# Kernel tuning notes

Hardware: AMD Instinct MI355X
Metric: run time of the kernel (lower is better)

## Reference

```python
import jax, jax.numpy as jnp
import numpy as np

N = 50000
E = 800000
NODE_IN, EDGE_IN, HID, OUT, L = 32, 16, 128, 128, 2


def _layer_norm(h, g, b, eps=1e-5):
    mu = jnp.mean(h, axis=-1, keepdims=True)
    var = jnp.var(h, axis=-1, keepdims=True)
    return (h - mu) * jax.lax.rsqrt(var + eps) * g + b


def setup_inputs() -> dict:
    key = jax.random.key(0)
    ks = jax.random.split(key, 20)
    s = lambda k, shape, fan: jax.random.normal(k, shape, jnp.float32) * (1.0 / np.sqrt(fan))
    return {
        "x": jax.random.normal(ks[0], (N, NODE_IN), jnp.float32),
        "edge_index": jax.random.randint(ks[1], (2, E), 0, N, jnp.int64),
        "edge_attr": jax.random.normal(ks[2], (E, EDGE_IN), jnp.float32),
        "enc_W": s(ks[3], (NODE_IN, HID), NODE_IN),
        "enc_b": jnp.zeros((HID,), jnp.float32),
        "enc_g": jnp.ones((HID,), jnp.float32),
        "enc_beta": jnp.zeros((HID,), jnp.float32),
        "msg_W1": s(ks[4], (L, 2 * HID + EDGE_IN, HID), 2 * HID + EDGE_IN),
        "msg_b1": jnp.zeros((L, HID), jnp.float32),
        "msg_W2": s(ks[5], (L, HID, HID), HID),
        "msg_b2": jnp.zeros((L, HID), jnp.float32),
        "upd_W1": s(ks[6], (L, 2 * HID, HID), 2 * HID),
        "upd_b1": jnp.zeros((L, HID), jnp.float32),
        "upd_W2": s(ks[7], (L, HID, HID), HID),
        "upd_b2": jnp.zeros((L, HID), jnp.float32),
        "ln_g": jnp.ones((L, HID), jnp.float32),
        "ln_beta": jnp.zeros((L, HID), jnp.float32),
        "head_W": s(ks[8], (HID, OUT), HID),
        "head_b": jnp.zeros((OUT,), jnp.float32),
    }


def reference(x, edge_index, edge_attr, enc_W, enc_b, enc_g, enc_beta,
              msg_W1, msg_b1, msg_W2, msg_b2, upd_W1, upd_b1, upd_W2, upd_b2,
              ln_g, ln_beta, head_W, head_b):
    src = edge_index[0]  # x_j (source)
    tgt = edge_index[1]  # x_i (target, aggregation index)
    n = x.shape[0]

    # node encoder: Linear -> ReLU -> LayerNorm
    h = jax.nn.relu(x @ enc_W + enc_b)
    h = _layer_norm(h, enc_g, enc_beta)

    # per-edge incoming-degree for mean aggregation (isolated nodes -> 0)
    cnt = jax.ops.segment_sum(jnp.ones((tgt.shape[0],), h.dtype), tgt, num_segments=n)
    denom = jnp.maximum(cnt, 1.0)[:, None]

    for l in range(L):
        x_i = h[tgt]                                 # [E, HID]
        x_j = h[src]                                 # [E, HID]
        msg_in = jnp.concatenate([x_i, x_j, edge_attr], axis=-1)  # [E, 2H+Ed]
        m = jax.nn.relu(msg_in @ msg_W1[l] + msg_b1[l]) @ msg_W2[l] + msg_b2[l]
        aggr = jax.ops.segment_sum(m, tgt, num_segments=n) / denom  # mean
        upd_in = jnp.concatenate([h, aggr], axis=-1)
        out = jax.nn.relu(upd_in @ upd_W1[l] + upd_b1[l]) @ upd_W2[l] + upd_b2[l]
        h = _layer_norm(h + out, ln_g[l], ln_beta[l])

    return h @ head_W + head_b
```

## Files before the change

kernel.cpp:

```cpp
#include <hip/hip_runtime.h>
#include <hip/hip_bf16.h>
#include <stdint.h>

#define N_NODES 50000
#define N_EDGES 800000
#define NL 2

#define KS2 136
#define KSU 264
#define ESTR 132

typedef __bf16 bf16x8 __attribute__((ext_vector_type(8)));
typedef float f32x4 __attribute__((ext_vector_type(4)));

__device__ __forceinline__ f32x4 mfma_bf16(uint4 a, uint4 b, f32x4 c) {
    return __builtin_amdgcn_mfma_f32_16x16x32_bf16(
        __builtin_bit_cast(bf16x8, a), __builtin_bit_cast(bf16x8, b), c, 0, 0, 0);
}

__device__ __forceinline__ unsigned short f2b(float f) {
    union { float f; unsigned u; } v; v.f = f;
    unsigned r = v.u + 0x7FFFu + ((v.u >> 16) & 1u);
    return (unsigned short)(r >> 16);
}

__device__ __forceinline__ float b2f(unsigned short u) {
    union { unsigned u; float f; } v; v.u = ((unsigned)u) << 16; return v.f;
}
__device__ __forceinline__ float b2f_lo(unsigned u) {
    union { unsigned u; float f; } v; v.u = u << 16; return v.f;
}
__device__ __forceinline__ float b2f_hi(unsigned u) {
    union { unsigned u; float f; } v; v.u = u & 0xFFFF0000u; return v.f;
}
__device__ __forceinline__ unsigned pk2(unsigned short a, unsigned short b) {
    return (unsigned)a | ((unsigned)b << 16);
}

template<int KSTEPS, int BSTR>
__device__ __forceinline__ void gemm4(const unsigned short* aLane,
                                      const unsigned short* bLane, f32x4 acc[4]) {
#pragma unroll
    for (int kc = 0; kc < KSTEPS; kc++) {
        uint4 a = *(const uint4*)(aLane + kc * 32);
#pragma unroll
        for (int ct = 0; ct < 4; ct++) {
            uint4 b = *(const uint4*)(bLane + (size_t)ct * 16 * BSTR + kc * 32);
            acc[ct] = mfma_bf16(a, b, acc[ct]);
        }
    }
}

template<int KSTEPS, int ASTR, int BSTR>
__device__ __forceinline__ void gemm_1x4(const unsigned short* aLane,
                                         const unsigned short* bLane,
                                         f32x4 acc[4]) {
#pragma unroll
    for (int kc = 0; kc < KSTEPS; kc++) {
        uint4 b0 = *(const uint4*)(bLane + kc * 32);
#pragma unroll
        for (int rt = 0; rt < 4; rt++) {
            uint4 a = *(const uint4*)(aLane + (size_t)rt * 16 * ASTR + kc * 32);
            acc[rt] = mfma_bf16(a, b0, acc[rt]);
        }
    }
}

template<int KSTEPS, int ASTR, int BSTR>
__device__ __forceinline__ void gemm_2x4(const unsigned short* aLane,
                                         const unsigned short* bLane,
                                         f32x4 acc[4][2]) {
#pragma unroll
    for (int kc = 0; kc < KSTEPS; kc++) {
        uint4 b0 = *(const uint4*)(bLane + kc * 32);
        uint4 b1 = *(const uint4*)(bLane + (size_t)16 * BSTR + kc * 32);
#pragma unroll
        for (int rt = 0; rt < 4; rt++) {
            uint4 a = *(const uint4*)(aLane + (size_t)rt * 16 * ASTR + kc * 32);
            acc[rt][0] = mfma_bf16(a, b0, acc[rt][0]);
            acc[rt][1] = mfma_bf16(a, b1, acc[rt][1]);
        }
    }
}

__global__ void prep_kernel(const float* __restrict__ mW1,
                            const float* __restrict__ uW1, const float* __restrict__ uW2,
                            const float* __restrict__ hW,
                            unsigned short* __restrict__ wab, unsigned short* __restrict__ w1cp,
                            unsigned short* __restrict__ u1t, unsigned short* __restrict__ u2t,
                            unsigned short* __restrict__ ht) {
    int i = blockIdx.x * 256 + threadIdx.x;
    const int SA = NL * 256 * 136;
    const int SC = NL * 128 * 32;
    const int SU = NL * 128 * KSU;
    const int S3 = NL * 128 * KS2;
    const int S4 = 128 * KS2;
    if (i < SA) {
        int l = i / (256 * 136), r = i % (256 * 136), j = r / 136, k = r % 136;
        float v = 0.f;
        if (k < 128)
            v = (j < 128) ? mW1[((size_t)l * 272 + k) * 128 + j]
                          : mW1[((size_t)l * 272 + 128 + k) * 128 + (j - 128)];
        wab[i] = f2b(v);
        return;
    }
    i -= SA;
    if (i < SC) {
        int l = i / (128 * 32), r = i % (128 * 32), j = r / 32, k = r % 32;
        w1cp[i] = (k < 16) ? f2b(mW1[((size_t)l * 272 + 256 + k) * 128 + j]) : (unsigned short)0;
        return;
    }
    i -= SC;
    if (i < SU) {
        int l = i / (128 * KSU), r = i % (128 * KSU), n = r / KSU, k = r % KSU;
        if (k < 128)       u1t[i] = f2b(uW1[((size_t)l * 256 + k) * 128 + n]);
        else if (k >= 256) u1t[i] = 0;
        return;
    }
    i -= SU;
    if (i < S3) {
        int l = i / (128 * KS2), r = i % (128 * KS2), n = r / KS2, k = r % KS2;
        u2t[i] = (k < 128) ? f2b(uW2[((size_t)l * 128 + k) * 128 + n]) : (unsigned short)0;
        return;
    }
    i -= S3;
    if (i < S4) {
        int n = i / KS2, k = i % KS2;
        ht[i] = (k < 128) ? f2b(hW[(size_t)k * 128 + n]) : (unsigned short)0;
    }
}

__global__ void prep2_kernel(const float* __restrict__ mW2, const float* __restrict__ uW1,
                             unsigned short* __restrict__ u1t) {
    __shared__ float w2row[128];
    const int l = blockIdx.x >> 7, j = blockIdx.x & 127;
    const int n = threadIdx.x;
    w2row[n] = mW2[((size_t)l * 128 + j) * 128 + n];
    __syncthreads();
    float s = 0.f;
#pragma unroll 8
    for (int c = 0; c < 128; c++)
        s += w2row[c] * uW1[((size_t)l * 256 + 128 + c) * 128 + n];
    u1t[(size_t)l * 128 * KSU + (size_t)n * KSU + 128 + j] = f2b(s);
}

__global__ void prep3_kernel(const float* __restrict__ mb2, const float* __restrict__ uW1,
                             float* __restrict__ bfold) {
    const int l = blockIdx.x;
    const int n = threadIdx.x;
    float s = 0.f;
#pragma unroll 8
    for (int c = 0; c < 128; c++)
        s += mb2[l * 128 + c] * uW1[((size_t)l * 256 + 128 + c) * 128 + n];
    bfold[l * 128 + n] = s;
}

__global__ __launch_bounds__(512, 6) void encnode_kernel(
        const float* __restrict__ x, const float* __restrict__ W,
        const float* __restrict__ b, const float* __restrict__ g, const float* __restrict__ bet,
        const unsigned short* __restrict__ wab, const float* __restrict__ b1,
        unsigned short* __restrict__ hb,
        unsigned short* __restrict__ Tb, unsigned short* __restrict__ Sb) {
    __shared__ __align__(16) unsigned short Ah[64 * KS2];
    __shared__ float xs[64 * 33];
    __shared__ __align__(16) float Ws[32 * 128];
    const int t = threadIdx.x;
    const int n0 = blockIdx.x * 64;

    {
        const int m = t >> 3, q = t & 7;
        const int nd = n0 + m;
        float4 v = {0.f, 0.f, 0.f, 0.f};
        if (nd < N_NODES) v = *(const float4*)(x + (size_t)nd * 32 + q * 4);
        xs[m * 33 + q * 4 + 0] = v.x;
        xs[m * 33 + q * 4 + 1] = v.y;
        xs[m * 33 + q * 4 + 2] = v.z;
        xs[m * 33 + q * 4 + 3] = v.w;
    }
    {
        const float4* s = (const float4*)W;
        float4* d = (float4*)Ws;
        d[t * 2] = s[t * 2];
        d[t * 2 + 1] = s[t * 2 + 1];
    }
    __syncthreads();

    const int r = t >> 3, q8 = t & 7;
    const int node = n0 + r;
    const bool valid = (node < N_NODES);

    float vbuf[16];
#pragma unroll
    for (int j = 0; j < 16; j++) vbuf[j] = b[q8 + 8 * j];
    for (int k = 0; k < 32; k++) {
        const float xv = xs[r * 33 + k];
#pragma unroll
        for (int j = 0; j < 16; j++)
            vbuf[j] += xv * Ws[k * 128 + q8 + 8 * j];
    }
#pragma unroll
    for (int j = 0; j < 16; j++) vbuf[j] = fmaxf(vbuf[j], 0.f);

    {
        float s = 0.f, ss = 0.f;
#pragma unroll
        for (int j = 0; j < 16; j++) { s += vbuf[j]; ss += vbuf[j] * vbuf[j]; }
        s += __shfl_xor(s, 1); ss += __shfl_xor(ss, 1);
        s += __shfl_xor(s, 2); ss += __shfl_xor(ss, 2);
        s += __shfl_xor(s, 4); ss += __shfl_xor(ss, 4);
        const float mu = s * (1.0f / 128.0f);
        const float var = ss * (1.0f / 128.0f) - mu * mu;
        const float rs = rsqrtf(var + 1e-5f);
#pragma unroll
        for (int j = 0; j < 16; j++) {
            const int col = q8 + 8 * j;
            const float v = (vbuf[j] - mu) * rs * g[col] + bet[col];
            Ah[r * KS2 + col] = valid ? f2b(v) : (unsigned short)0;
        }
    }
    __syncthreads();

    {
        const int m = t >> 3, q = t & 7;
        const int nd = n0 + m;
        if (nd < N_NODES) {
            const uint4* srow = (const uint4*)(Ah + (size_t)m * KS2);
            uint4* drow = (uint4*)(hb + (size_t)nd * 128);
            drow[q * 2] = srow[q * 2];
            drow[q * 2 + 1] = srow[q * 2 + 1];
        }
    }

    const int wv = t >> 6, lane = t & 63, lr = lane & 15, lq = lane >> 4;
    const int cbn = wv * 32;
    const f32x4 z4 = {0.f, 0.f, 0.f, 0.f};
    f32x4 accn[4][2];
#pragma unroll
    for (int i = 0; i < 4; i++) { accn[i][0] = z4; accn[i][1] = z4; }
    gemm_2x4<4, KS2, KS2>(Ah + lr * KS2 + lq * 8,
                          wab + (size_t)(cbn + lr) * KS2 + lq * 8, accn);
#pragma unroll
    for (int ct = 0; ct < 2; ct++) {
        const int j = cbn + ct * 16 + lr;
        const float bias = (j < 128) ? b1[j] : 0.f;
#pragma unroll
        for (int rt = 0; rt < 4; rt++) {
#pragma unroll
            for (int r2 = 0; r2 < 4; r2++) {
                const int node2 = n0 + rt * 16 + lq * 4 + r2;
                if (node2 < N_NODES) {
                    const float v = accn[rt][ct][r2] + bias;
                    if (j < 128) Tb[(size_t)node2 * 128 + j] = f2b(v);
                    else         Sb[(size_t)node2 * 128 + (j - 128)] = f2b(v);
                }
            }
        }
    }
}

__global__ void hist_kernel(const int* __restrict__ tgt, int* __restrict__ hist) {
    int i = blockIdx.x * 256 + threadIdx.x;
    atomicAdd(hist + tgt[i], 1);
}

__global__ void scan1_kernel(const int* __restrict__ hist, int* __restrict__ incl,
                             int* __restrict__ blksum) {
    __shared__ int buf[256];
    const int t = threadIdx.x;
    const int i = blockIdx.x * 256 + t;
    int v = (i < N_NODES) ? hist[i] : 0;
    buf[t] = v; __syncthreads();
#pragma unroll
    for (int d = 1; d < 256; d <<= 1) {
        int x = (t >= d) ? buf[t - d] : 0;
        __syncthreads();
        buf[t] += x;
        __syncthreads();
    }
    if (i < N_NODES) incl[i] = buf[t];
    if (t == 255) blksum[blockIdx.x] = buf[255];
}

__global__ void scan2_kernel(int* __restrict__ blksum, int nblk) {
    __shared__ int buf[256];
    const int t = threadIdx.x;
    int v = (t < nblk) ? blksum[t] : 0;
    buf[t] = v; __syncthreads();
#pragma unroll
    for (int d = 1; d < 256; d <<= 1) {
        int x = (t >= d) ? buf[t - d] : 0;
        __syncthreads();
        buf[t] += x;
        __syncthreads();
    }
    if (t < nblk) blksum[t] = buf[t];
}

__global__ void scan3_kernel(int* __restrict__ incl, const int* __restrict__ blksum,
                             const int* __restrict__ hist) {
    const int i = blockIdx.x * 256 + threadIdx.x;
    if (i >= N_NODES) return;
    const int b = blockIdx.x;
    const int base = (b > 0) ? blksum[b - 1] : 0;
    incl[i] = incl[i] + base - hist[i];
}

__global__ void scatterp_kernel(const int* __restrict__ src, const int* __restrict__ tgt,
                                int* __restrict__ cursor, uint2* __restrict__ permst) {
    const int e = blockIdx.x * 256 + threadIdx.x;
    const int tg = tgt[e];
    const int p = atomicAdd(cursor + tg, 1);
    permst[p] = make_uint2((unsigned)e, ((unsigned)src[e] << 16) | (unsigned)tg);
}

__global__ __launch_bounds__(256) void gather_kernel(
        const uint2* __restrict__ permst, const float* __restrict__ ea,
        unsigned int* __restrict__ sST, unsigned short* __restrict__ eabS) {
    const int p = blockIdx.x * 256 + threadIdx.x;
    const uint2 v = permst[p];
    sST[p] = v.y;
    const float4* s = (const float4*)(ea + (size_t)v.x * 16);
    ushort4* d = (ushort4*)(eabS + (size_t)p * 16);
#pragma unroll
    for (int i = 0; i < 4; i++) {
        float4 f = s[i];
        d[i] = make_ushort4(f2b(f.x), f2b(f.y), f2b(f.z), f2b(f.w));
    }
}

__global__ __launch_bounds__(256, 8) void edge_kernel(
        const unsigned short* __restrict__ eabS,
        const unsigned int* __restrict__ sST,
        const unsigned short* __restrict__ w1cp,
        const unsigned short* __restrict__ Tb, const unsigned short* __restrict__ Sb,
        float* __restrict__ aggr) {
    __shared__ __align__(16) float Es[32 * ESTR];
    __shared__ int sT[64];
    __shared__ int sS[64];

    const int t = threadIdx.x;
    const int e0 = blockIdx.x * 64;
    if (t < 64) {
        const unsigned v = sST[e0 + t];
        sT[t] = (int)(v & 0xFFFFu);
        sS[t] = (int)(v >> 16);
    }
    __syncthreads();

    const int wv = t >> 6, lane = t & 63, lr = lane & 15, lq = lane >> 4;
    const int rtw = (wv >> 1) * 16;
    const int cbw = (wv & 1) * 64;
    const int m = t & 31, c8b = t >> 5;
    const f32x4 z4 = {0.f, 0.f, 0.f, 0.f};

    unsigned long long bmask;
    {
        const int l = t & 63;
        const int a = sT[l];
        const int b = (l > 0) ? sT[l - 1] : a;
        bmask = __ballot(a != b);
    }

    uint4 t0a, t0b, s0a, s0b;
    {
        const unsigned short* Tr = Tb + (size_t)sT[m] * 128;
        const unsigned short* Sr = Sb + (size_t)sS[m] * 128;
        t0a = *(const uint4*)(Tr + c8b * 8);
        t0b = *(const uint4*)(Tr + c8b * 8 + 64);
        s0a = *(const uint4*)(Sr + c8b * 8);
        s0b = *(const uint4*)(Sr + c8b * 8 + 64);
    }

    float s = 0.f;
    bool first = true;

    {
        uint4 a = {0, 0, 0, 0};
        if (lq < 2)
            a = *(const uint4*)(eabS + (size_t)(e0 + rtw + lr) * 16 + lq * 8);
        f32x4 acc[4];
#pragma unroll
        for (int ct = 0; ct < 4; ct++) {
            uint4 b = *(const uint4*)(w1cp + (cbw + ct * 16 + lr) * 32 + lq * 8);
            acc[ct] = mfma_bf16(a, b, z4);
        }
#pragma unroll
        for (int ct = 0; ct < 4; ct++) {
            const int col = cbw + ct * 16 + lr;
#pragma unroll
            for (int r = 0; r < 4; r++)
                Es[(rtw + lq * 4 + r) * ESTR + col] = acc[ct][r];
        }
    }
    __syncthreads();

    uint4 t1a, t1b, s1a, s1b;
    {
        float* Erow = Es + m * ESTR;
        float4* EA = (float4*)(Erow + c8b * 8);
        float4* EB = (float4*)(Erow + c8b * 8 + 64);
        float4 ea0 = EA[0], ea1 = EA[1];
        ea0.x = fmaxf(ea0.x + b2f_lo(t0a.x) + b2f_lo(s0a.x), 0.f);
        ea0.y = fmaxf(ea0.y + b2f_hi(t0a.x) + b2f_hi(s0a.x), 0.f);
        ea0.z = fmaxf(ea0.z + b2f_lo(t0a.y) + b2f_lo(s0a.y), 0.f);
        ea0.w = fmaxf(ea0.w + b2f_hi(t0a.y) + b2f_hi(s0a.y), 0.f);
        ea1.x = fmaxf(ea1.x + b2f_lo(t0a.z) + b2f_lo(s0a.z), 0.f);
        ea1.y = fmaxf(ea1.y + b2f_hi(t0a.z) + b2f_hi(s0a.z), 0.f);
        ea1.z = fmaxf(ea1.z + b2f_lo(t0a.w) + b2f_lo(s0a.w), 0.f);
        ea1.w = fmaxf(ea1.w + b2f_hi(t0a.w) + b2f_hi(s0a.w), 0.f);
        EA[0] = ea0; EA[1] = ea1;
        float4 eb0 = EB[0], eb1 = EB[1];
        eb0.x = fmaxf(eb0.x + b2f_lo(t0b.x) + b2f_lo(s0b.x), 0.f);
        eb0.y = fmaxf(eb0.y + b2f_hi(t0b.x) + b2f_hi(s0b.x), 0.f);
        eb0.z = fmaxf(eb0.z + b2f_lo(t0b.y) + b2f_lo(s0b.y), 0.f);
        eb0.w = fmaxf(eb0.w + b2f_hi(t0b.y) + b2f_hi(s0b.y), 0.f);
        eb1.x = fmaxf(eb1.x + b2f_lo(t0b.z) + b2f_lo(s0b.z), 0.f);
        eb1.y = fmaxf(eb1.y + b2f_hi(t0b.z) + b2f_hi(s0b.z), 0.f);
        eb1.z = fmaxf(eb1.z + b2f_lo(t0b.w) + b2f_lo(s0b.w), 0.f);
        eb1.w = fmaxf(eb1.w + b2f_hi(t0b.w) + b2f_hi(s0b.w), 0.f);
        EB[0] = eb0; EB[1] = eb1;

        const unsigned short* Tr = Tb + (size_t)sT[32 + m] * 128;
        const unsigned short* Sr = Sb + (size_t)sS[32 + m] * 128;
        t1a = *(const uint4*)(Tr + c8b * 8);
        t1b = *(const uint4*)(Tr + c8b * 8 + 64);
        s1a = *(const uint4*)(Sr + c8b * 8);
        s1b = *(const uint4*)(Sr + c8b * 8 + 64);
    }
    __syncthreads();

    if (t < 128) {
        const int c = t;
        const unsigned mh = (unsigned)bmask;
#pragma unroll
        for (int i8 = 0; i8 < 4; i8++) {
            float v[8];
#pragma unroll
            for (int j = 0; j < 8; j++) v[j] = Es[(i8 * 8 + j) * ESTR + c];
#pragma unroll
            for (int j = 0; j < 8; j++) {
                const int i = i8 * 8 + j;
                if (mh & (1u << i)) {
                    float* dst = aggr + (size_t)sT[i - 1] * 128 + c;
                    if (first) { atomicAdd(dst, s); first = false; }
                    else       { *dst = s; }
                    s = 0.f;
                }
                s += v[j];
            }
        }
    }
    __syncthreads();

    {
        uint4 a = {0, 0, 0, 0};
        if (lq < 2)
            a = *(const uint4*)(eabS + (size_t)(e0 + 32 + rtw + lr) * 16 + lq * 8);
        f32x4 acc[4];
#pragma unroll
        for (int ct = 0; ct < 4; ct++) {
            uint4 b = *(const uint4*)(w1cp + (cbw + ct * 16 + lr) * 32 + lq * 8);
            acc[ct] = mfma_bf16(a, b, z4);
        }
#pragma unroll
        for (int ct = 0; ct < 4; ct++) {
            const int col = cbw + ct * 16 + lr;
#pragma unroll
            for (int r = 0; r < 4; r++)
                Es[(rtw + lq * 4 + r) * ESTR + col] = acc[ct][r];
        }
    }
    __syncthreads();

    {
        float* Erow = Es + m * ESTR;
        float4* EA = (float4*)(Erow + c8b * 8);
        float4* EB = (float4*)(Erow + c8b * 8 + 64);
        float4 ea0 = EA[0], ea1 = EA[1];
        ea0.x = fmaxf(ea0.x + b2f_lo(t1a.x) + b2f_lo(s1a.x), 0.f);
        ea0.y = fmaxf(ea0.y + b2f_hi(t1a.x) + b2f_hi(s1a.x), 0.f);
        ea0.z = fmaxf(ea0.z + b2f_lo(t1a.y) + b2f_lo(s1a.y), 0.f);
        ea0.w = fmaxf(ea0.w + b2f_hi(t1a.y) + b2f_hi(s1a.y), 0.f);
        ea1.x = fmaxf(ea1.x + b2f_lo(t1a.z) + b2f_lo(s1a.z), 0.f);
        ea1.y = fmaxf(ea1.y + b2f_hi(t1a.z) + b2f_hi(s1a.z), 0.f);
        ea1.z = fmaxf(ea1.z + b2f_lo(t1a.w) + b2f_lo(s1a.w), 0.f);
        ea1.w = fmaxf(ea1.w + b2f_hi(t1a.w) + b2f_hi(s1a.w), 0.f);
        EA[0] = ea0; EA[1] = ea1;
        float4 eb0 = EB[0], eb1 = EB[1];
        eb0.x = fmaxf(eb0.x + b2f_lo(t1b.x) + b2f_lo(s1b.x), 0.f);
        eb0.y = fmaxf(eb0.y + b2f_hi(t1b.x) + b2f_hi(s1b.x), 0.f);
        eb0.z = fmaxf(eb0.z + b2f_lo(t1b.y) + b2f_lo(s1b.y), 0.f);
        eb0.w = fmaxf(eb0.w + b2f_hi(t1b.y) + b2f_hi(s1b.y), 0.f);
        eb1.x = fmaxf(eb1.x + b2f_lo(t1b.z) + b2f_lo(s1b.z), 0.f);
        eb1.y = fmaxf(eb1.y + b2f_hi(t1b.z) + b2f_hi(s1b.z), 0.f);
        eb1.z = fmaxf(eb1.z + b2f_lo(t1b.w) + b2f_lo(s1b.w), 0.f);
        eb1.w = fmaxf(eb1.w + b2f_hi(t1b.w) + b2f_hi(s1b.w), 0.f);
        EB[0] = eb0; EB[1] = eb1;
    }
    __syncthreads();

    if (t < 128) {
        const int c = t;
        const unsigned mh = (unsigned)(bmask >> 32);
#pragma unroll
        for (int i8 = 0; i8 < 4; i8++) {
            float v[8];
#pragma unroll
            for (int j = 0; j < 8; j++) v[j] = Es[(i8 * 8 + j) * ESTR + c];
#pragma unroll
            for (int j = 0; j < 8; j++) {
                const int i = i8 * 8 + j;
                if (mh & (1u << i)) {
                    float* dst = aggr + (size_t)sT[32 + i - 1] * 128 + c;
                    if (first) { atomicAdd(dst, s); first = false; }
                    else       { *dst = s; }
                    s = 0.f;
                }
                s += v[j];
            }
        }
        atomicAdd(aggr + (size_t)sT[63] * 128 + c, s);
    }
}

__global__ __launch_bounds__(512, 6) void upd_kernel(
        const unsigned short* __restrict__ hb_in,
        const float* __restrict__ aggr, const int* __restrict__ hist,
        const unsigned short* __restrict__ u1t, const unsigned short* __restrict__ u2t,
        const float* __restrict__ b1, const float* __restrict__ bf,
        const float* __restrict__ b2,
        const float* __restrict__ g, const float* __restrict__ bet,
        unsigned short* __restrict__ hb_out,
        const unsigned short* __restrict__ wabn, const float* __restrict__ b1n,
        unsigned short* __restrict__ Tb, unsigned short* __restrict__ Sb,
        const unsigned short* __restrict__ ht, const float* __restrict__ hbias,
        float* __restrict__ out, const int mode) {
    __shared__ __align__(16) char smemA[64 * KSU * 2];
    __shared__ float sF[64];
    unsigned short* As = (unsigned short*)smemA;
    float* LNb = (float*)smemA;

    const int t = threadIdx.x;
    const int n0 = blockIdx.x * 64;
    {
        const int m = t >> 3, q = t & 7;
        const int node = n0 + m;
        unsigned short* row = As + m * KSU;
        if (node < N_NODES) {
            const uint4* ph = (const uint4*)(hb_in + (size_t)node * 128);
            uint4* d0 = (uint4*)row;
            d0[q * 2] = ph[q * 2];
            d0[q * 2 + 1] = ph[q * 2 + 1];
            const int cntv = hist[node];
            if (q == 0) sF[m] = (cntv > 0) ? 1.f : 0.f;
            const float rden = 1.0f / fmaxf((float)cntv, 1.0f);
            const float4* pa = (const float4*)(aggr + (size_t)node * 128 + q * 16);
            ushort4* d1 = (ushort4*)(row + 128 + q * 16);
#pragma unroll
            for (int i = 0; i < 4; i++) {
                float4 v = pa[i];
                d1[i] = make_ushort4(f2b(v.x * rden), f2b(v.y * rden),
                                     f2b(v.z * rden), f2b(v.w * rden));
            }
            if (q == 0) { uint4 z{0, 0, 0, 0}; ((uint4*)(row + 256))[0] = z; }
        } else {
            if (q == 0) sF[m] = 0.f;
            uint4 z{0, 0, 0, 0};
            uint4* d = (uint4*)row;
            for (int i = q; i < 33; i += 8) d[i] = z;
        }
    }
    __syncthreads();

    const int wv = t >> 6, lane = t & 63, lr = lane & 15, lq = lane >> 4;
    const int cb16 = wv * 16;
    const f32x4 z4 = {0.f, 0.f, 0.f, 0.f};

    f32x4 acc[4];
#pragma unroll
    for (int i = 0; i < 4; i++) acc[i] = z4;
    gemm_1x4<8, KSU, KSU>(As + lr * KSU + lq * 8,
                          u1t + (size_t)(cb16 + lr) * KSU + lq * 8, acc);
    __syncthreads();

    {
        const int col = cb16 + lr;
        const float bv = b1[col];
        const float bfv = bf[col];
#pragma unroll
        for (int rt = 0; rt < 4; rt++) {
#pragma unroll
            for (int r = 0; r < 4; r++) {
                const int ml = rt * 16 + lq * 4 + r;
                float v = fmaxf(acc[rt][r] + bv + sF[ml] * bfv, 0.f);
                As[ml * KSU + 128 + col] = f2b(v);
            }
        }
    }
    __syncthreads();

    f32x4 acc2[4];
#pragma unroll
    for (int i = 0; i < 4; i++) acc2[i] = z4;
    gemm_1x4<4, KSU, KS2>(As + lr * KSU + 128 + lq * 8,
                          u2t + (size_t)(cb16 + lr) * KS2 + lq * 8, acc2);
    __syncthreads();

    float hres[4][4];
    {
        const int colr = cb16 + lr;
#pragma unroll
        for (int rt = 0; rt < 4; rt++)
#pragma unroll
            for (int r = 0; r < 4; r++)
                hres[rt][r] = b2f(As[(rt * 16 + lq * 4 + r) * KSU + colr]);
    }
    __syncthreads();

    {
        const int col = cb16 + lr;
        const float bv = b2[col];
#pragma unroll
        for (int rt = 0; rt < 4; rt++) {
#pragma unroll
            for (int r = 0; r < 4; r++) {
                const int ml = rt * 16 + lq * 4 + r;
                LNb[ml * 132 + col] = acc2[rt][r] + bv + hres[rt][r];
            }
        }
    }
    __syncthreads();

    const int r = t >> 3, c0 = (t & 7) * 16;
    const int node = n0 + r;
    const bool valid = (node < N_NODES);
    float vbuf[16];
    if (valid) {
        float s = 0.f, ss = 0.f;
#pragma unroll
        for (int i = 0; i < 16; i++) {
            const float v = LNb[r * 132 + c0 + i];
            vbuf[i] = v;
            s += v; ss += v * v;
        }
        s += __shfl_xor(s, 1); ss += __shfl_xor(ss, 1);
        s += __shfl_xor(s, 2); ss += __shfl_xor(ss, 2);
        s += __shfl_xor(s, 4); ss += __shfl_xor(ss, 4);
        const float mu = s * (1.0f / 128.0f);
        const float var = ss * (1.0f / 128.0f) - mu * mu;
        const float rs = rsqrtf(var + 1e-5f);
#pragma unroll
        for (int i = 0; i < 16; i++) {
            const int j = c0 + i;
            vbuf[i] = (vbuf[i] - mu) * rs * g[j] + bet[j];
        }
    }
    __syncthreads();

    unsigned short* Ah = (unsigned short*)smemA;
    {
        unsigned short hb16[16];
#pragma unroll
        for (int i = 0; i < 16; i++) hb16[i] = valid ? f2b(vbuf[i]) : (unsigned short)0;
        uint4* arow = (uint4*)(Ah + (size_t)r * KS2 + c0);
#pragma unroll
        for (int k8 = 0; k8 < 2; k8++)
            arow[k8] = make_uint4(pk2(hb16[k8 * 8 + 0], hb16[k8 * 8 + 1]),
                                  pk2(hb16[k8 * 8 + 2], hb16[k8 * 8 + 3]),
                                  pk2(hb16[k8 * 8 + 4], hb16[k8 * 8 + 5]),
                                  pk2(hb16[k8 * 8 + 6], hb16[k8 * 8 + 7]));
        if (mode == 2 && valid) {
            uint4* drow = (uint4*)(hb_out + (size_t)node * 128 + c0);
#pragma unroll
            for (int k8 = 0; k8 < 2; k8++)
                drow[k8] = make_uint4(pk2(hb16[k8 * 8 + 0], hb16[k8 * 8 + 1]),
                                      pk2(hb16[k8 * 8 + 2], hb16[k8 * 8 + 3]),
                                      pk2(hb16[k8 * 8 + 4], hb16[k8 * 8 + 5]),
                                      pk2(hb16[k8 * 8 + 6], hb16[k8 * 8 + 7]));
        }
    }
    __syncthreads();

    if (mode == 1) {
        const int m0 = (wv & 3) * 16;
        const int cblk = (wv >> 2) * 64;
        f32x4 hacc[4];
#pragma unroll
        for (int i = 0; i < 4; i++) hacc[i] = z4;
        gemm4<4, KS2>(Ah + (size_t)(m0 + lr) * KS2 + lq * 8,
                      ht + (size_t)(cblk + lr) * KS2 + lq * 8, hacc);
#pragma unroll
        for (int ct = 0; ct < 4; ct++) {
            const int col = cblk + ct * 16 + lr;
            const float bv = hbias[col];
#pragma unroll
            for (int r2 = 0; r2 < 4; r2++) {
                const int node2 = n0 + m0 + lq * 4 + r2;
                if (node2 < N_NODES) out[(size_t)node2 * 128 + col] = hacc[ct][r2] + bv;
            }
        }
    } else {
        const int cbn = wv * 32;
        f32x4 accn[4][2];
#pragma unroll
        for (int i = 0; i < 4; i++) { accn[i][0] = z4; accn[i][1] = z4; }
        gemm_2x4<4, KS2, KS2>(Ah + lr * KS2 + lq * 8,
                              wabn + (size_t)(cbn + lr) * KS2 + lq * 8, accn);
#pragma unroll
        for (int ct = 0; ct < 2; ct++) {
            const int j = cbn + ct * 16 + lr;
            const float bias = (j < 128) ? b1n[j] : 0.f;
#pragma unroll
            for (int rt = 0; rt < 4; rt++) {
#pragma unroll
                for (int r2 = 0; r2 < 4; r2++) {
                    const int node2 = n0 + rt * 16 + lq * 4 + r2;
                    if (node2 < N_NODES) {
                        const float v = accn[rt][ct][r2] + bias;
                        if (j < 128) Tb[(size_t)node2 * 128 + j] = f2b(v);
                        else         Sb[(size_t)node2 * 128 + (j - 128)] = f2b(v);
                    }
                }
            }
        }
    }
}

extern "C" void kernel_launch(void* const* d_in, const int* in_sizes, int n_in,
                              void* d_out, int out_size, void* d_ws, size_t ws_size,
                              hipStream_t stream) {
    const float* x       = (const float*)d_in[0];
    const int*   ei      = (const int*)d_in[1];
    const float* ea      = (const float*)d_in[2];
    const float* encW    = (const float*)d_in[3];
    const float* encb    = (const float*)d_in[4];
    const float* encg    = (const float*)d_in[5];
    const float* encbeta = (const float*)d_in[6];
    const float* msgW1   = (const float*)d_in[7];
    const float* msgb1   = (const float*)d_in[8];
    const float* msgW2   = (const float*)d_in[9];
    const float* msgb2   = (const float*)d_in[10];
    const float* updW1   = (const float*)d_in[11];
    const float* updb1   = (const float*)d_in[12];
    const float* updW2   = (const float*)d_in[13];
    const float* updb2   = (const float*)d_in[14];
    const float* lng     = (const float*)d_in[15];
    const float* lnbeta  = (const float*)d_in[16];
    const float* headW   = (const float*)d_in[17];
    const float* headb   = (const float*)d_in[18];

    char* w = (char*)d_ws;
    size_t off = 0;
    auto nxt = [&](size_t bytes) -> void* {
        void* p = w + off;
        off = (off + bytes + 255) & ~(size_t)255;
        return p;
    };
    unsigned short* hb    = (unsigned short*)nxt((size_t)N_NODES * 128 * 2);
    float*          aggr  = (float*)nxt((size_t)N_NODES * 128 * 4);
    unsigned short* Tb    = (unsigned short*)nxt((size_t)N_NODES * 128 * 2);
    unsigned short* Sb    = (unsigned short*)nxt((size_t)N_NODES * 128 * 2);
    unsigned short* eabS  = (unsigned short*)nxt((size_t)N_EDGES * 16 * 2);
    unsigned int*   sST   = (unsigned int*)nxt((size_t)N_EDGES * 4);
    int*            hist  = (int*)nxt((size_t)N_NODES * 4);
    int*            incl  = (int*)nxt((size_t)N_NODES * 4);
    int*            blksum= (int*)nxt(256 * 4);
    unsigned short* wab   = (unsigned short*)nxt((size_t)NL * 256 * 136 * 2);
    unsigned short* w1cp  = (unsigned short*)nxt((size_t)NL * 128 * 32 * 2);
    unsigned short* u1t   = (unsigned short*)nxt((size_t)NL * 128 * KSU * 2);
    unsigned short* u2t   = (unsigned short*)nxt((size_t)NL * 128 * KS2 * 2);
    unsigned short* ht    = (unsigned short*)nxt((size_t)128 * KS2 * 2);
    float*          bfold = (float*)nxt((size_t)NL * 128 * 4);

    uint2*          permst = (uint2*)aggr;

    const int NBLK = (N_NODES + 255) / 256;
    const int PREP_N = NL * 256 * 136 + NL * 128 * 32 + NL * 128 * KSU
                     + NL * 128 * KS2 + 128 * KS2;

    hipMemsetAsync(hist, 0, (size_t)N_NODES * 4, stream);
    prep_kernel<<<(PREP_N + 255) / 256, 256, 0, stream>>>(msgW1, updW1, updW2, headW,
                                                          wab, w1cp, u1t, u2t, ht);
    prep2_kernel<<<NL * 128, 128, 0, stream>>>(msgW2, updW1, u1t);
    prep3_kernel<<<NL, 128, 0, stream>>>(msgb2, updW1, bfold);
    encnode_kernel<<<782, 512, 0, stream>>>(x, encW, encb, encg, encbeta,
                                            wab, msgb1, hb, Tb, Sb);
    hist_kernel<<<3125, 256, 0, stream>>>(ei + N_EDGES, hist);
    scan1_kernel<<<NBLK, 256, 0, stream>>>(hist, incl, blksum);
    scan2_kernel<<<1, 256, 0, stream>>>(blksum, NBLK);
    scan3_kernel<<<NBLK, 256, 0, stream>>>(incl, blksum, hist);
    scatterp_kernel<<<3125, 256, 0, stream>>>(ei, ei + N_EDGES, incl, permst);
    gather_kernel<<<3125, 256, 0, stream>>>(permst, ea, sST, eabS);

    for (int l = 0; l < NL; l++) {
        hipMemsetAsync(aggr, 0, (size_t)N_NODES * 128 * 4, stream);
        edge_kernel<<<12500, 256, 0, stream>>>(eabS, sST,
                                               w1cp + (size_t)l * 128 * 32,
                                               Tb, Sb, aggr);
        upd_kernel<<<782, 512, 0, stream>>>(hb, aggr, hist,
                                            u1t + (size_t)l * 128 * KSU,
                                            u2t + (size_t)l * 128 * KS2,
                                            updb1 + l * 128, bfold + l * 128,
                                            updb2 + l * 128,
                                            lng + l * 128, lnbeta + l * 128,
                                            hb,
                                            wab + (size_t)(l + 1 < NL ? l + 1 : 0) * 256 * 136,
                                            msgb1 + (l + 1 < NL ? l + 1 : 0) * 128,
                                            Tb, Sb,
                                            ht, headb, (float*)d_out,
                                            (l == NL - 1) ? 1 : 2);
    }
}
```

Measured before the change: 500.4 us.

## Keep node state in fp32 and halve node tile to 32 rows per block

The node hidden state buffer moves from bf16 to fp32, so the residual add in the update LayerNorm uses full-precision h held in registers rather than a bf16 copy read back from shared memory. Node kernels now process 32 nodes per 512-thread block instead of 64, which doubles the grid and reduces shared memory per block so more blocks fit per CU. In exchange, the h buffer traffic doubles and each block does less MFMA work against the same weight loads, lowering weight reuse.

New measurement: 478.7 us (median of 2 runs). 4.3% less time.

```diff
diff --git a/kernel.cpp b/kernel.cpp
--- a/kernel.cpp
+++ b/kernel.cpp
@@ -24,9 +24,6 @@
     return (unsigned short)(r >> 16);
 }
 
-__device__ __forceinline__ float b2f(unsigned short u) {
-    union { unsigned u; float f; } v; v.u = ((unsigned)u) << 16; return v.f;
-}
 __device__ __forceinline__ float b2f_lo(unsigned u) {
     union { unsigned u; float f; } v; v.u = u << 16; return v.f;
 }
@@ -37,45 +34,31 @@
     return (unsigned)a | ((unsigned)b << 16);
 }
 
-template<int KSTEPS, int BSTR>
-__device__ __forceinline__ void gemm4(const unsigned short* aLane,
-                                      const unsigned short* bLane, f32x4 acc[4]) {
-#pragma unroll
-    for (int kc = 0; kc < KSTEPS; kc++) {
-        uint4 a = *(const uint4*)(aLane + kc * 32);
-#pragma unroll
-        for (int ct = 0; ct < 4; ct++) {
-            uint4 b = *(const uint4*)(bLane + (size_t)ct * 16 * BSTR + kc * 32);
-            acc[ct] = mfma_bf16(a, b, acc[ct]);
-        }
-    }
-}
-
-template<int KSTEPS, int ASTR, int BSTR>
-__device__ __forceinline__ void gemm_1x4(const unsigned short* aLane,
+template<int RT, int KSTEPS, int ASTR, int BSTR>
+__device__ __forceinline__ void gemm_1xR(const unsigned short* aLane,
                                          const unsigned short* bLane,
-                                         f32x4 acc[4]) {
+                                         f32x4 acc[RT]) {
 #pragma unroll
     for (int kc = 0; kc < KSTEPS; kc++) {
         uint4 b0 = *(const uint4*)(bLane + kc * 32);
 #pragma unroll
-        for (int rt = 0; rt < 4; rt++) {
+        for (int rt = 0; rt < RT; rt++) {
             uint4 a = *(const uint4*)(aLane + (size_t)rt * 16 * ASTR + kc * 32);
             acc[rt] = mfma_bf16(a, b0, acc[rt]);
         }
     }
 }
 
-template<int KSTEPS, int ASTR, int BSTR>
-__device__ __forceinline__ void gemm_2x4(const unsigned short* aLane,
+template<int RT, int KSTEPS, int ASTR, int BSTR>
+__device__ __forceinline__ void gemm_2xR(const unsigned short* aLane,
                                          const unsigned short* bLane,
-                                         f32x4 acc[4][2]) {
+                                         f32x4 acc[RT][2]) {
 #pragma unroll
     for (int kc = 0; kc < KSTEPS; kc++) {
         uint4 b0 = *(const uint4*)(bLane + kc * 32);
         uint4 b1 = *(const uint4*)(bLane + (size_t)16 * BSTR + kc * 32);
 #pragma unroll
-        for (int rt = 0; rt < 4; rt++) {
+        for (int rt = 0; rt < RT; rt++) {
             uint4 a = *(const uint4*)(aLane + (size_t)rt * 16 * ASTR + kc * 32);
             acc[rt][0] = mfma_bf16(a, b0, acc[rt][0]);
             acc[rt][1] = mfma_bf16(a, b1, acc[rt][1]);
@@ -155,27 +138,25 @@
     bfold[l * 128 + n] = s;
 }
 
-__global__ __launch_bounds__(512, 6) void encnode_kernel(
+__global__ __launch_bounds__(512, 8) void encnode_kernel(
         const float* __restrict__ x, const float* __restrict__ W,
         const float* __restrict__ b, const float* __restrict__ g, const float* __restrict__ bet,
         const unsigned short* __restrict__ wab, const float* __restrict__ b1,
-        unsigned short* __restrict__ hb,
+        float* __restrict__ h,
         unsigned short* __restrict__ Tb, unsigned short* __restrict__ Sb) {
-    __shared__ __align__(16) unsigned short Ah[64 * KS2];
-    __shared__ float xs[64 * 33];
+    __shared__ __align__(16) unsigned short Ah[32 * KS2];
+    __shared__ float xs[32 * 33];
     __shared__ __align__(16) float Ws[32 * 128];
     const int t = threadIdx.x;
-    const int n0 = blockIdx.x * 64;
-
-    {
-        const int m = t >> 3, q = t & 7;
+    const int n0 = blockIdx.x * 32;
+
+    {
+        const int m = t >> 4, q = t & 15;
         const int nd = n0 + m;
-        float4 v = {0.f, 0.f, 0.f, 0.f};
-        if (nd < N_NODES) v = *(const float4*)(x + (size_t)nd * 32 + q * 4);
-        xs[m * 33 + q * 4 + 0] = v.x;
-        xs[m * 33 + q * 4 + 1] = v.y;
-        xs[m * 33 + q * 4 + 2] = v.z;
-        xs[m * 33 + q * 4 + 3] = v.w;
+        float2 v = {0.f, 0.f};
+        if (nd < N_NODES) v = *(const float2*)(x + (size_t)nd * 32 + q * 2);
+        xs[m * 33 + q * 2 + 0] = v.x;
+        xs[m * 33 + q * 2 + 1] = v.y;
     }
     {
         const float4* s = (const float4*)W;
@@ -185,66 +166,57 @@
     }
     __syncthreads();
 
-    const int r = t >> 3, q8 = t & 7;
+    const int r = t >> 4, q16 = t & 15;
     const int node = n0 + r;
     const bool valid = (node < N_NODES);
 
-    float vbuf[16];
-#pragma unroll
-    for (int j = 0; j < 16; j++) vbuf[j] = b[q8 + 8 * j];
+    float vbuf[8];
+#pragma unroll
+    for (int j = 0; j < 8; j++) vbuf[j] = b[q16 + 16 * j];
     for (int k = 0; k < 32; k++) {
         const float xv = xs[r * 33 + k];
 #pragma unroll
-        for (int j = 0; j < 16; j++)
-            vbuf[j] += xv * Ws[k * 128 + q8 + 8 * j];
-    }
-#pragma unroll
-    for (int j = 0; j < 16; j++) vbuf[j] = fmaxf(vbuf[j], 0.f);
+        for (int j = 0; j < 8; j++)
+            vbuf[j] += xv * Ws[k * 128 + q16 + 16 * j];
+    }
+#pragma unroll
+    for (int j = 0; j < 8; j++) vbuf[j] = fmaxf(vbuf[j], 0.f);
 
     {
         float s = 0.f, ss = 0.f;
 #pragma unroll
-        for (int j = 0; j < 16; j++) { s += vbuf[j]; ss += vbuf[j] * vbuf[j]; }
+        for (int j = 0; j < 8; j++) { s += vbuf[j]; ss += vbuf[j] * vbuf[j]; }
         s += __shfl_xor(s, 1); ss += __shfl_xor(ss, 1);
         s += __shfl_xor(s, 2); ss += __shfl_xor(ss, 2);
         s += __shfl_xor(s, 4); ss += __shfl_xor(ss, 4);
+        s += __shfl_xor(s, 8); ss += __shfl_xor(ss, 8);
         const float mu = s * (1.0f / 128.0f);
         const float var = ss * (1.0f / 128.0f) - mu * mu;
         const float rs = rsqrtf(var + 1e-5f);
 #pragma unroll
-        for (int j = 0; j < 16; j++) {
-            const int col = q8 + 8 * j;
+        for (int j = 0; j < 8; j++) {
+            const int col = q16 + 16 * j;
             const float v = (vbuf[j] - mu) * rs * g[col] + bet[col];
             Ah[r * KS2 + col] = valid ? f2b(v) : (unsigned short)0;
-        }
-    }
-    __syncthreads();
-
-    {
-        const int m = t >> 3, q = t & 7;
-        const int nd = n0 + m;
-        if (nd < N_NODES) {
-            const uint4* srow = (const uint4*)(Ah + (size_t)m * KS2);
-            uint4* drow = (uint4*)(hb + (size_t)nd * 128);
-            drow[q * 2] = srow[q * 2];
-            drow[q * 2 + 1] = srow[q * 2 + 1];
-        }
-    }
+            if (valid) h[(size_t)node * 128 + col] = v;
+        }
+    }
+    __syncthreads();
 
     const int wv = t >> 6, lane = t & 63, lr = lane & 15, lq = lane >> 4;
     const int cbn = wv * 32;
     const f32x4 z4 = {0.f, 0.f, 0.f, 0.f};
-    f32x4 accn[4][2];
-#pragma unroll
-    for (int i = 0; i < 4; i++) { accn[i][0] = z4; accn[i][1] = z4; }
-    gemm_2x4<4, KS2, KS2>(Ah + lr * KS2 + lq * 8,
-                          wab + (size_t)(cbn + lr) * KS2 + lq * 8, accn);
+    f32x4 accn[2][2];
+#pragma unroll
+    for (int i = 0; i < 2; i++) { accn[i][0] = z4; accn[i][1] = z4; }
+    gemm_2xR<2, 4, KS2, KS2>(Ah + lr * KS2 + lq * 8,
+                             wab + (size_t)(cbn + lr) * KS2 + lq * 8, accn);
 #pragma unroll
     for (int ct = 0; ct < 2; ct++) {
         const int j = cbn + ct * 16 + lr;
         const float bias = (j < 128) ? b1[j] : 0.f;
 #pragma unroll
-        for (int rt = 0; rt < 4; rt++) {
+        for (int rt = 0; rt < 2; rt++) {
 #pragma unroll
             for (int r2 = 0; r2 < 4; r2++) {
                 const int node2 = n0 + rt * 16 + lq * 4 + r2;
@@ -523,41 +495,47 @@
     }
 }
 
-__global__ __launch_bounds__(512, 6) void upd_kernel(
-        const unsigned short* __restrict__ hb_in,
+__global__ __launch_bounds__(512, 8) void upd_kernel(
+        const float* __restrict__ h_in,
         const float* __restrict__ aggr, const int* __restrict__ hist,
         const unsigned short* __restrict__ u1t, const unsigned short* __restrict__ u2t,
         const float* __restrict__ b1, const float* __restrict__ bf,
         const float* __restrict__ b2,
         const float* __restrict__ g, const float* __restrict__ bet,
-        unsigned short* __restrict__ hb_out,
+        float* __restrict__ h_out,
         const unsigned short* __restrict__ wabn, const float* __restrict__ b1n,
         unsigned short* __restrict__ Tb, unsigned short* __restrict__ Sb,
         const unsigned short* __restrict__ ht, const float* __restrict__ hbias,
         float* __restrict__ out, const int mode) {
-    __shared__ __align__(16) char smemA[64 * KSU * 2];
-    __shared__ float sF[64];
+    __shared__ __align__(16) char smemA[32 * KSU * 2];
+    __shared__ float sF[32];
     unsigned short* As = (unsigned short*)smemA;
     float* LNb = (float*)smemA;
 
     const int t = threadIdx.x;
-    const int n0 = blockIdx.x * 64;
-    {
-        const int m = t >> 3, q = t & 7;
+    const int n0 = blockIdx.x * 32;
+    float hrv[8];
+#pragma unroll
+    for (int i = 0; i < 8; i++) hrv[i] = 0.f;
+    {
+        const int m = t >> 4, q = t & 15;
         const int node = n0 + m;
         unsigned short* row = As + m * KSU;
         if (node < N_NODES) {
-            const uint4* ph = (const uint4*)(hb_in + (size_t)node * 128);
-            uint4* d0 = (uint4*)row;
-            d0[q * 2] = ph[q * 2];
-            d0[q * 2 + 1] = ph[q * 2 + 1];
+            const float4* ph = (const float4*)(h_in + (size_t)node * 128 + q * 8);
+            const float4 h0 = ph[0], h1 = ph[1];
+            hrv[0] = h0.x; hrv[1] = h0.y; hrv[2] = h0.z; hrv[3] = h0.w;
+            hrv[4] = h1.x; hrv[5] = h1.y; hrv[6] = h1.z; hrv[7] = h1.w;
+            ((uint4*)(row + q * 8))[0] =
+                make_uint4(pk2(f2b(hrv[0]), f2b(hrv[1])), pk2(f2b(hrv[2]), f2b(hrv[3])),
+                           pk2(f2b(hrv[4]), f2b(hrv[5])), pk2(f2b(hrv[6]), f2b(hrv[7])));
             const int cntv = hist[node];
             if (q == 0) sF[m] = (cntv > 0) ? 1.f : 0.f;
             const float rden = 1.0f / fmaxf((float)cntv, 1.0f);
-            const float4* pa = (const float4*)(aggr + (size_t)node * 128 + q * 16);
-            ushort4* d1 = (ushort4*)(row + 128 + q * 16);
-#pragma unroll
-            for (int i = 0; i < 4; i++) {
+            const float4* pa = (const float4*)(aggr + (size_t)node * 128 + q * 8);
+            ushort4* d1 = (ushort4*)(row + 128 + q * 8);
+#pragma unroll
+            for (int i = 0; i < 2; i++) {
                 float4 v = pa[i];
                 d1[i] = make_ushort4(f2b(v.x * rden), f2b(v.y * rden),
                                      f2b(v.z * rden), f2b(v.w * rden));
@@ -567,7 +545,7 @@
             if (q == 0) sF[m] = 0.f;
             uint4 z{0, 0, 0, 0};
             uint4* d = (uint4*)row;
-            for (int i = q; i < 33; i += 8) d[i] = z;
+            for (int i = q; i < 33; i += 16) d[i] = z;
         }
     }
     __syncthreads();
@@ -576,11 +554,10 @@
     const int cb16 = wv * 16;
     const f32x4 z4 = {0.f, 0.f, 0.f, 0.f};
 
-    f32x4 acc[4];
-#pragma unroll
-    for (int i = 0; i < 4; i++) acc[i] = z4;
-    gemm_1x4<8, KSU, KSU>(As + lr * KSU + lq * 8,
-                          u1t + (size_t)(cb16 + lr) * KSU + lq * 8, acc);
+    f32x4 acc[2];
+    acc[0] = z4; acc[1] = z4;
+    gemm_1xR<2, 8, KSU, KSU>(As + lr * KSU + lq * 8,
+                             u1t + (size_t)(cb16 + lr) * KSU + lq * 8, acc);
     __syncthreads();
 
     {
@@ -588,7 +565,7 @@
         const float bv = b1[col];
         const float bfv = bf[col];
 #pragma unroll
-        for (int rt = 0; rt < 4; rt++) {
+        for (int rt = 0; rt < 2; rt++) {
 #pragma unroll
             for (int r = 0; r < 4; r++) {
                 const int ml = rt * 16 + lq * 4 + r;
@@ -599,58 +576,47 @@
     }
     __syncthreads();
 
-    f32x4 acc2[4];
-#pragma unroll
-    for (int i = 0; i < 4; i++) acc2[i] = z4;
-    gemm_1x4<4, KSU, KS2>(As + lr * KSU + 128 + lq * 8,
-                          u2t + (size_t)(cb16 + lr) * KS2 + lq * 8, acc2);
-    __syncthreads();
-
-    float hres[4][4];
-    {
-        const int colr = cb16 + lr;
-#pragma unroll
-        for (int rt = 0; rt < 4; rt++)
-#pragma unroll
-            for (int r = 0; r < 4; r++)
-                hres[rt][r] = b2f(As[(rt * 16 + lq * 4 + r) * KSU + colr]);
-    }
+    f32x4 acc2[2];
+    acc2[0] = z4; acc2[1] = z4;
+    gemm_1xR<2, 4, KSU, KS2>(As + lr * KSU + 128 + lq * 8,
+                             u2t + (size_t)(cb16 + lr) * KS2 + lq * 8, acc2);
     __syncthreads();
 
     {
         const int col = cb16 + lr;
         const float bv = b2[col];
 #pragma unroll
-        for (int rt = 0; rt < 4; rt++) {
+        for (int rt = 0; rt < 2; rt++) {
 #pragma unroll
             for (int r = 0; r < 4; r++) {
                 const int ml = rt * 16 + lq * 4 + r;
-                LNb[ml * 132 + col] = acc2[rt][r] + bv + hres[rt][r];
+                LNb[ml * 132 + col] = acc2[rt][r] + bv;
             }
         }
     }
     __syncthreads();
 
-    const int r = t >> 3, c0 = (t & 7) * 16;
+    const int r = t >> 4, c0 = (t & 15) * 8;
     const int node = n0 + r;
     const bool valid = (node < N_NODES);
-    float vbuf[16];
+    float vbuf[8];
     if (valid) {
         float s = 0.f, ss = 0.f;
 #pragma unroll
-        for (int i = 0; i < 16; i++) {
-            const float v = LNb[r * 132 + c0 + i];
+        for (int i = 0; i < 8; i++) {
+            const float v = LNb[r * 132 + c0 + i] + hrv[i];
             vbuf[i] = v;
             s += v; ss += v * v;
         }
         s += __shfl_xor(s, 1); ss += __shfl_xor(ss, 1);
         s += __shfl_xor(s, 2); ss += __shfl_xor(ss, 2);
         s += __shfl_xor(s, 4); ss += __shfl_xor(ss, 4);
+        s += __shfl_xor(s, 8); ss += __shfl_xor(ss, 8);
         const float mu = s * (1.0f / 128.0f);
         const float var = ss * (1.0f / 128.0f) - mu * mu;
         const float rs = rsqrtf(var + 1e-5f);
 #pragma unroll
-        for (int i = 0; i < 16; i++) {
+        for (int i = 0; i < 8; i++) {
             const int j = c0 + i;
             vbuf[i] = (vbuf[i] - mu) * rs * g[j] + bet[j];
         }
@@ -659,59 +625,50 @@
 
     unsigned short* Ah = (unsigned short*)smemA;
     {
-        unsigned short hb16[16];
-#pragma unroll
-        for (int i = 0; i < 16; i++) hb16[i] = valid ? f2b(vbuf[i]) : (unsigned short)0;
+        unsigned short hb16[8];
+#pragma unroll
+        for (int i = 0; i < 8; i++) hb16[i] = valid ? f2b(vbuf[i]) : (unsigned short)0;
         uint4* arow = (uint4*)(Ah + (size_t)r * KS2 + c0);
-#pragma unroll
-        for (int k8 = 0; k8 < 2; k8++)
-            arow[k8] = make_uint4(pk2(hb16[k8 * 8 + 0], hb16[k8 * 8 + 1]),
-                                  pk2(hb16[k8 * 8 + 2], hb16[k8 * 8 + 3]),
-                                  pk2(hb16[k8 * 8 + 4], hb16[k8 * 8 + 5]),
-                                  pk2(hb16[k8 * 8 + 6], hb16[k8 * 8 + 7]));
+        arow[0] = make_uint4(pk2(hb16[0], hb16[1]), pk2(hb16[2], hb16[3]),
+                             pk2(hb16[4], hb16[5]), pk2(hb16[6], hb16[7]));
         if (mode == 2 && valid) {
-            uint4* drow = (uint4*)(hb_out + (size_t)node * 128 + c0);
-#pragma unroll
-            for (int k8 = 0; k8 < 2; k8++)
-                drow[k8] = make_uint4(pk2(hb16[k8 * 8 + 0], hb16[k8 * 8 + 1]),
-                                      pk2(hb16[k8 * 8 + 2], hb16[k8 * 8 + 3]),
-                                      pk2(hb16[k8 * 8 + 4], hb16[k8 * 8 + 5]),
-                                      pk2(hb16[k8 * 8 + 6], hb16[k8 * 8 + 7]));
+            float4* drow = (float4*)(h_out + (size_t)node * 128 + c0);
+            drow[0] = make_float4(vbuf[0], vbuf[1], vbuf[2], vbuf[3]);
+            drow[1] = make_float4(vbuf[4], vbuf[5], vbuf[6], vbuf[7]);
         }
     }
     __syncthreads();
 
     if (mode == 1) {
-        const int m0 = (wv & 3) * 16;
-        const int cblk = (wv >> 2) * 64;
-        f32x4 hacc[4];
-#pragma unroll
-        for (int i = 0; i < 4; i++) hacc[i] = z4;
-        gemm4<4, KS2>(Ah + (size_t)(m0 + lr) * KS2 + lq * 8,
-                      ht + (size_t)(cblk + lr) * KS2 + lq * 8, hacc);
-#pragma unroll
-        for (int ct = 0; ct < 4; ct++) {
+        const int m0 = (wv & 1) * 16;
+        const int cblk = (wv >> 1) * 32;
+        f32x4 hacc[1][2];
+        hacc[0][0] = z4; hacc[0][1] = z4;
+        gemm_2xR<1, 4, KS2, KS2>(Ah + (size_t)(m0 + lr) * KS2 + lq * 8,
+                                 ht + (size_t)(cblk + lr) * KS2 + lq * 8, hacc);
+#pragma unroll
+        for (int ct = 0; ct < 2; ct++) {
             const int col = cblk + ct * 16 + lr;
             const float bv = hbias[col];
 #pragma unroll
             for (int r2 = 0; r2 < 4; r2++) {
                 const int node2 = n0 + m0 + lq * 4 + r2;
-                if (node2 < N_NODES) out[(size_t)node2 * 128 + col] = hacc[ct][r2] + bv;
+                if (node2 < N_NODES) out[(size_t)node2 * 128 + col] = hacc[0][ct][r2] + bv;
             }
         }
     } else {
         const int cbn = wv * 32;
-        f32x4 accn[4][2];
-#pragma unroll
-        for (int i = 0; i < 4; i++) { accn[i][0] = z4; accn[i][1] = z4; }
-        gemm_2x4<4, KS2, KS2>(Ah + lr * KS2 + lq * 8,
-                              wabn + (size_t)(cbn + lr) * KS2 + lq * 8, accn);
+        f32x4 accn[2][2];
+#pragma unroll
+        for (int i = 0; i < 2; i++) { accn[i][0] = z4; accn[i][1] = z4; }
+        gemm_2xR<2, 4, KS2, KS2>(Ah + lr * KS2 + lq * 8,
+                                 wabn + (size_t)(cbn + lr) * KS2 + lq * 8, accn);
 #pragma unroll
         for (int ct = 0; ct < 2; ct++) {
             const int j = cbn + ct * 16 + lr;
             const float bias = (j < 128) ? b1n[j] : 0.f;
 #pragma unroll
-            for (int rt = 0; rt < 4; rt++) {
+            for (int rt = 0; rt < 2; rt++) {
 #pragma unroll
                 for (int r2 = 0; r2 < 4; r2++) {
                     const int node2 = n0 + rt * 16 + lq * 4 + r2;
@@ -756,7 +713,7 @@
         off = (off + bytes + 255) & ~(size_t)255;
         return p;
     };
-    unsigned short* hb    = (unsigned short*)nxt((size_t)N_NODES * 128 * 2);
+    float*          h     = (float*)nxt((size_t)N_NODES * 128 * 4);
     float*          aggr  = (float*)nxt((size_t)N_NODES * 128 * 4);
     unsigned short* Tb    = (unsigned short*)nxt((size_t)N_NODES * 128 * 2);
     unsigned short* Sb    = (unsigned short*)nxt((size_t)N_NODES * 128 * 2);
@@ -775,6 +732,7 @@
     uint2*          permst = (uint2*)aggr;
 
     const int NBLK = (N_NODES + 255) / 256;
+    const int NODEBLK = (N_NODES + 31) / 32;
     const int PREP_N = NL * 256 * 136 + NL * 128 * 32 + NL * 128 * KSU
                      + NL * 128 * KS2 + 128 * KS2;
 
@@ -783,8 +741,8 @@
                                                           wab, w1cp, u1t, u2t, ht);
     prep2_kernel<<<NL * 128, 128, 0, stream>>>(msgW2, updW1, u1t);
     prep3_kernel<<<NL, 128, 0, stream>>>(msgb2, updW1, bfold);
-    encnode_kernel<<<782, 512, 0, stream>>>(x, encW, encb, encg, encbeta,
-                                            wab, msgb1, hb, Tb, Sb);
+    encnode_kernel<<<NODEBLK, 512, 0, stream>>>(x, encW, encb, encg, encbeta,
+                                                wab, msgb1, h, Tb, Sb);
     hist_kernel<<<3125, 256, 0, stream>>>(ei + N_EDGES, hist);
     scan1_kernel<<<NBLK, 256, 0, stream>>>(hist, incl, blksum);
     scan2_kernel<<<1, 256, 0, stream>>>(blksum, NBLK);
@@ -797,13 +755,13 @@
         edge_kernel<<<12500, 256, 0, stream>>>(eabS, sST,
                                                w1cp + (size_t)l * 128 * 32,
                                                Tb, Sb, aggr);
-        upd_kernel<<<782, 512, 0, stream>>>(hb, aggr, hist,
+        upd_kernel<<<NODEBLK, 512, 0, stream>>>(h, aggr, hist,
                                             u1t + (size_t)l * 128 * KSU,
                                             u2t + (size_t)l * 128 * KS2,
                                             updb1 + l * 128, bfold + l * 128,
                                             updb2 + l * 128,
                                             lng + l * 128, lnbeta + l * 128,
-                                            hb,
+                                            h,
                                             wab + (size_t)(l + 1 < NL ? l + 1 : 0) * 256 * 136,
                                             msgb1 + (l + 1 < NL ? l + 1 : 0) * 128,
                                             Tb, Sb,
```
